# Kernel optimization log

Hardware: AMD Instinct MI355X
Metric: run time of the kernel (lower is better)

The kernel has to match this reference:

```python
import jax, jax.numpy as jnp
import numpy as np

B, V = 4, 5                      # batch_size, nview
CUBE = (80, 80, 20)              # PICT_STRUCT.CUBE_SIZE
NBINS = CUBE[0] * CUBE[1] * CUBE[2]
IMG_W, IMG_H = 960, 512          # NETWORK.IMAGE_SIZE (w, h)
ORI_W, ORI_H = 1920, 1080        # NETWORK.ORI_IMAGE_SIZE
HM_W, HM_H = 240, 128            # NETWORK.HEATMAP_SIZE
C_IMG, C_FEAT = 3, 32
C_TOT = C_IMG + C_FEAT
HID = 256
D_IN = 3 + 2 * C_TOT             # points + [mean, var] volume features


def setup_inputs():
    key = jax.random.key(0)
    ks = jax.random.split(key, 10)
    denorm_imgs = jax.random.uniform(ks[0], (V, B, C_IMG, IMG_H, IMG_W), jnp.float32)
    feats2d = jax.random.normal(ks[1], (V, B, C_FEAT, HM_H, HM_W), jnp.float32)
    lo = jnp.array([-1500.0, -1500.0, -300.0], jnp.float32)
    hi = jnp.array([1500.0, 1500.0, 300.0], jnp.float32)
    grids = lo + (hi - lo) * jax.random.uniform(ks[2], (B, NBINS, 3), jnp.float32)
    # near-identity rotations, camera centers ~3m behind the volume so all
    # points project inside the original image
    R = jnp.tile(jnp.eye(3, dtype=jnp.float32), (V, B, 1, 1)) \
        + 0.01 * jax.random.normal(ks[3], (V, B, 3, 3), jnp.float32)
    T = jnp.tile(jnp.array([0.0, 0.0, -3000.0], jnp.float32).reshape(3, 1), (V, B, 1, 1)) \
        + 50.0 * jax.random.normal(ks[4], (V, B, 3, 1), jnp.float32)
    f = 1500.0 + 10.0 * jax.random.normal(ks[5], (V, B, 2), jnp.float32)
    c_cam = jnp.tile(jnp.array([ORI_W / 2.0, ORI_H / 2.0], jnp.float32), (V, B, 1))
    k_dist = jnp.zeros((V, B, 3), jnp.float32)
    p_dist = jnp.zeros((V, B, 2), jnp.float32)
    resize_transform = jnp.array([[IMG_W / ORI_W, 0.0, 0.0],
                                  [0.0, IMG_H / ORI_H, 0.0]], jnp.float32)
    s1, s2 = 1.0 / np.sqrt(D_IN), 1.0 / np.sqrt(HID)
    W1 = (s1 * jax.random.normal(ks[6], (D_IN, HID))).astype(jnp.float32)
    b1 = jnp.zeros((HID,), jnp.float32)
    W2 = (s2 * jax.random.normal(ks[7], (HID, HID))).astype(jnp.float32)
    b2 = jnp.zeros((HID,), jnp.float32)
    W3 = (s2 * jax.random.normal(ks[8], (HID, 1))).astype(jnp.float32)
    b3 = jnp.zeros((1,), jnp.float32)
    return dict(denorm_imgs=denorm_imgs, feats2d=feats2d, grids=grids, R=R, T=T,
                f=f, c_cam=c_cam, k_dist=k_dist, p_dist=p_dist,
                resize_transform=resize_transform,
                W1=W1, b1=b1, W2=W2, b2=b2, W3=W3, b3=b3)


def _project(x, R, T, f, c, k, p):
    # voxelpose project_point_radial: x [N,3] world-mm -> [N,2] pixel coords
    xcam = R @ (x.T - T)                               # [3,N]
    y = xcam[:2] / (xcam[2:3] + 1e-5)                  # [2,N]
    r2 = jnp.sum(y * y, axis=0)
    radial = 1.0 + k[0] * r2 + k[1] * r2 ** 2 + k[2] * r2 ** 3
    tan = p[0] * y[1] + p[1] * y[0]
    y = y * (radial + 2.0 * tan)[None, :] + jnp.stack([p[1], p[0]])[:, None] * r2[None, :]
    return (f[:, None] * y + c[:, None]).T             # [N,2]


def _bilinear(img, gx, gy):
    # F.grid_sample bilinear, align_corners=True, padding_mode='zeros'
    # img: [C,H,W]; gx,gy: [N] in [-1,1] -> [C,N]
    C, H, W = img.shape
    x = (gx + 1.0) * 0.5 * (W - 1)
    y = (gy + 1.0) * 0.5 * (H - 1)
    x0, y0 = jnp.floor(x), jnp.floor(y)
    wx1, wy1 = x - x0, y - y0
    wx0, wy0 = 1.0 - wx1, 1.0 - wy1

    def tap(xi, yi):
        valid = (xi >= 0) & (xi <= W - 1) & (yi >= 0) & (yi <= H - 1)
        xi_c = jnp.clip(xi.astype(jnp.int32), 0, W - 1)
        yi_c = jnp.clip(yi.astype(jnp.int32), 0, H - 1)
        return img[:, yi_c, xi_c] * valid.astype(img.dtype)

    return (tap(x0, y0) * (wx0 * wy0) + tap(x0 + 1.0, y0) * (wx1 * wy0)
            + tap(x0, y0 + 1.0) * (wx0 * wy1) + tap(x0 + 1.0, y0 + 1.0) * (wx1 * wy1))


def _sample_view(img, feat, pts, R, T, f, c, k, p, trans):
    xy = _project(pts, R, T, f, c, k, p)
    xy = jnp.clip(xy, -1.0, float(max(ORI_W, ORI_H)))
    xy = jnp.concatenate([xy, jnp.ones((xy.shape[0], 1), xy.dtype)], axis=1) @ trans.T
    g = xy / jnp.array([IMG_W - 1.0, IMG_H - 1.0], jnp.float32) * 2.0 - 1.0
    si = _bilinear(img, g[:, 0], g[:, 1])              # [C_IMG, N]
    sf = _bilinear(feat, g[:, 0], g[:, 1])             # [C_FEAT, N]
    return jnp.concatenate([si, sf], axis=0)           # [C_TOT, N]


def reference(denorm_imgs, feats2d, grids, R, T, f, c_cam, k_dist, p_dist,
              resize_transform, W1, b1, W2, b2, W3, b3):
    per_b = jax.vmap(_sample_view, in_axes=(0, 0, 0, 0, 0, 0, 0, 0, 0, None))
    per_vb = jax.vmap(per_b, in_axes=(0, 0, None, 0, 0, 0, 0, 0, 0, None))
    cubes = per_vb(denorm_imgs, feats2d, grids, R, T, f, c_cam, k_dist, p_dist,
                   resize_transform)                   # [V,B,C,N]
    cubes = jnp.transpose(cubes, (1, 2, 3, 0))         # [B,C,N,V]
    mean = jnp.mean(cubes, axis=-1)                    # sum(cubes/nview)
    var = jnp.sum((cubes - mean[..., None]) ** 2, axis=-1) / V
    var = jnp.exp(-var)
    gvol = jnp.concatenate([mean, var], axis=1)        # [B,2C,N]
    # nerf_model.query_density: MLP over (points, per-point global volume feats)
    feat = jnp.concatenate([grids / 1000.0, jnp.swapaxes(gvol, 1, 2)], axis=-1)  # [B,N,D_IN]
    h = jax.nn.relu(feat @ W1 + b1)
    h = jax.nn.relu(h @ W2 + b2)
    density = jax.nn.softplus(h @ W3 + b3)             # [B,N,1]
    alpha = 1.0 - jnp.exp(-density)
    return alpha.reshape(B, 1, CUBE[0], CUBE[1], CUBE[2])
```

## Files before the change

### kernel.cpp

```cpp
#include <hip/hip_runtime.h>

#define NVIEW 5
#define BATCH 4
#define NPTS 128000
#define CIMG 3
#define CFEAT 32
#define CTOT 35
#define DIN 73
#define HID 256
#define IMG_W 960
#define IMG_H 512
#define HM_W 240
#define HM_H 128
#define HW_IMG (IMG_W * IMG_H)
#define HW_HM (HM_W * HM_H)

#define BP 32

typedef __attribute__((ext_vector_type(8))) short bf16x8;
typedef __attribute__((ext_vector_type(4))) float f32x4;
typedef __attribute__((ext_vector_type(4))) unsigned short ushort4v;
typedef __attribute__((ext_vector_type(8))) unsigned short ushort8v;

__device__ inline unsigned short bf16_rtne(float f) {
    unsigned u = __builtin_bit_cast(unsigned, f);
    u += 0x7FFFu + ((u >> 16) & 1u);
    return (unsigned short)(u >> 16);
}

struct Tap {
    int o00, o01, o10, o11;
    float w00, w01, w10, w11;
};

__device__ inline void make_tap(float gx, float gy, int W, int H, Tap& t) {
    float x = (gx + 1.0f) * 0.5f * (float)(W - 1);
    float y = (gy + 1.0f) * 0.5f * (float)(H - 1);
    float x0 = floorf(x), y0 = floorf(y);
    float x1 = x0 + 1.0f, y1 = y0 + 1.0f;
    float wx1 = x - x0, wy1 = y - y0;
    float wx0 = 1.0f - wx1, wy0 = 1.0f - wy1;
    float vx0 = (x0 >= 0.0f && x0 <= (float)(W - 1)) ? 1.0f : 0.0f;
    float vx1 = (x1 >= 0.0f && x1 <= (float)(W - 1)) ? 1.0f : 0.0f;
    float vy0 = (y0 >= 0.0f && y0 <= (float)(H - 1)) ? 1.0f : 0.0f;
    float vy1 = (y1 >= 0.0f && y1 <= (float)(H - 1)) ? 1.0f : 0.0f;
    int ix0 = min(max((int)x0, 0), W - 1);
    int ix1 = min(max((int)x1, 0), W - 1);
    int iy0 = min(max((int)y0, 0), H - 1);
    int iy1 = min(max((int)y1, 0), H - 1);
    t.o00 = iy0 * W + ix0;  t.w00 = wx0 * wy0 * vx0 * vy0;
    t.o01 = iy0 * W + ix1;  t.w01 = wx1 * wy0 * vx1 * vy0;
    t.o10 = iy1 * W + ix0;  t.w10 = wx0 * wy1 * vx0 * vy1;
    t.o11 = iy1 * W + ix1;  t.w11 = wx1 * wy1 * vx1 * vy1;
}

__device__ inline float4 f4zero() { float4 r; r.x = r.y = r.z = r.w = 0.f; return r; }
__device__ inline float4 f4fma(float w, float4 a, float4 acc) {
    acc.x += w * a.x; acc.y += w * a.y; acc.z += w * a.z; acc.w += w * a.w; return acc;
}
__device__ inline float4 f4add(float4 a, float4 b) {
    a.x += b.x; a.y += b.y; a.z += b.z; a.w += b.w; return a;
}
__device__ inline float4 f4addsq(float4 acc, float4 v) {
    acc.x += v.x * v.x; acc.y += v.y * v.y; acc.z += v.z * v.z; acc.w += v.w * v.w; return acc;
}

__global__ __launch_bounds__(256) void transpose_img(const float* __restrict__ in,
                                                     float* __restrict__ out) {
    int idx = blockIdx.x * 256 + threadIdx.x;
    int vb = idx / HW_IMG;
    int pix = idx - vb * HW_IMG;
    const float* src = in + (size_t)vb * 3 * HW_IMG + pix;
    float4 o;
    o.x = src[0];
    o.y = src[HW_IMG];
    o.z = src[2 * HW_IMG];
    o.w = 0.0f;
    reinterpret_cast<float4*>(out)[idx] = o;
}

__global__ __launch_bounds__(256) void transpose_feat(const float* __restrict__ in,
                                                      float* __restrict__ out) {
    int idx = blockIdx.x * 256 + threadIdx.x;
    int vb = idx / HW_HM;
    int pix = idx - vb * HW_HM;
    const float* src = in + (size_t)vb * 32 * HW_HM + pix;
    float4* dst = reinterpret_cast<float4*>(out) + (size_t)idx * 8;
#pragma unroll
    for (int k = 0; k < 8; ++k) {
        float4 o;
        o.x = src[(4 * k + 0) * HW_HM];
        o.y = src[(4 * k + 1) * HW_HM];
        o.z = src[(4 * k + 2) * HW_HM];
        o.w = src[(4 * k + 3) * HW_HM];
        dst[k] = o;
    }
}

__global__ __launch_bounds__(256) void prep_weights(const float* __restrict__ W1,
                                                    const float* __restrict__ W2,
                                                    unsigned short* __restrict__ W1b,
                                                    unsigned short* __restrict__ W2b) {
    int idx = blockIdx.x * 256 + threadIdx.x;
    if (idx < 16 * 3 * 64) {
        int l = idx & 63;
        int ks = (idx >> 6) % 3;
        int nt = idx / 192;
        int n = nt * 16 + (l & 15);
        int k0 = ks * 32 + (l >> 4) * 8;
        ushort8v o;
#pragma unroll
        for (int j = 0; j < 8; ++j) {
            int k = k0 + j;
            float v = (k < DIN) ? W1[k * HID + n] : 0.0f;
            o[j] = bf16_rtne(v);
        }
        reinterpret_cast<ushort8v*>(W1b)[idx] = o;
    } else if (idx < 16 * 3 * 64 + 16 * 8 * 64) {
        int id2 = idx - 16 * 3 * 64;
        int l = id2 & 63;
        int ks = (id2 >> 6) & 7;
        int nt = id2 >> 9;
        int n = nt * 16 + (l & 15);
        int k0 = ks * 32 + (l >> 4) * 8;
        ushort8v o;
#pragma unroll
        for (int j = 0; j < 8; ++j)
            o[j] = bf16_rtne(W2[(k0 + j) * HID + n]);
        reinterpret_cast<ushort8v*>(W2b)[id2] = o;
    }
}

__global__ __launch_bounds__(256, 4) void fused_denorm_project(
    const float* __restrict__ wsImg,
    const float* __restrict__ wsFeat,
    const unsigned short* __restrict__ W1b,
    const unsigned short* __restrict__ W2b,
    const float* __restrict__ grids,
    const float* __restrict__ Rm,
    const float* __restrict__ Tm,
    const float* __restrict__ fcam,
    const float* __restrict__ ccam,
    const float* __restrict__ kdist,
    const float* __restrict__ pdist,
    const float* __restrict__ trans,
    const float* __restrict__ b1,
    const float* __restrict__ b2,
    const float* __restrict__ W3,
    const float* __restrict__ b3,
    float* __restrict__ out)
{
    __shared__ unsigned short featb[BP * 96];
    __shared__ unsigned short h1T[BP * 256];
    __shared__ float b1L[HID], b2L[HID], w3L[HID];
    __shared__ float partial[4][BP];

    const int tid = threadIdx.x;
    const int blk = blockIdx.x;
    const int b   = blk / (NPTS / BP);
    const int n0  = (blk % (NPTS / BP)) * BP;

    b1L[tid] = b1[tid];
    b2L[tid] = b2[tid];
    w3L[tid] = W3[tid];

    {
        const int t = tid & 7;
        const int p = tid >> 3;
        const int n = n0 + p;
        char* fbB = (char*)featb;
        const int rowoff = p * 192;
        const int sw = (p & 7) << 4;

        const float px = grids[(b * NPTS + n) * 3 + 0];
        const float py = grids[(b * NPTS + n) * 3 + 1];
        const float pz = grids[(b * NPTS + n) * 3 + 2];
        if (t == 1) {
            *(unsigned short*)(fbB + ((rowoff + 0) ^ sw)) = bf16_rtne(px * 1e-3f);
            *(unsigned short*)(fbB + ((rowoff + 2) ^ sw)) = bf16_rtne(py * 1e-3f);
            *(unsigned short*)(fbB + ((rowoff + 4) ^ sw)) = bf16_rtne(pz * 1e-3f);
        }
        {
            int c0 = 73 + t * 3;
            int cnt = (t == 7) ? 2 : 3;
            for (int j = 0; j < cnt; ++j)
                *(unsigned short*)(fbB + ((rowoff + (c0 + j) * 2) ^ sw)) = 0;
        }
        const float t00 = trans[0], t01 = trans[1], t02 = trans[2];
        const float t10 = trans[3], t11 = trans[4], t12 = trans[5];

        float4 s4 = f4zero(), q4 = f4zero();
        float4 si = f4zero(), qi = f4zero();

        for (int v = 0; v < NVIEW; ++v) {
            const int vb = v * BATCH + b;
            const float* Rp = Rm + vb * 9;
            const float* Tp = Tm + vb * 3;
            float X = px - Tp[0], Y = py - Tp[1], Z = pz - Tp[2];
            float xc = Rp[0] * X + Rp[1] * Y + Rp[2] * Z;
            float yc = Rp[3] * X + Rp[4] * Y + Rp[5] * Z;
            float zc = Rp[6] * X + Rp[7] * Y + Rp[8] * Z;
            float inv = 1.0f / (zc + 1e-5f);
            float y0 = xc * inv, y1 = yc * inv;
            float r2 = y0 * y0 + y1 * y1;
            float k0 = kdist[vb * 3 + 0], k1 = kdist[vb * 3 + 1], k2 = kdist[vb * 3 + 2];
            float p0 = pdist[vb * 2 + 0], p1 = pdist[vb * 2 + 1];
            float radial = 1.0f + r2 * (k0 + r2 * (k1 + r2 * k2));
            float tn = p0 * y1 + p1 * y0;
            float scl = radial + 2.0f * tn;
            float uu = y0 * scl + p1 * r2;
            float vv = y1 * scl + p0 * r2;
            float xo = fcam[vb * 2 + 0] * uu + ccam[vb * 2 + 0];
            float yo = fcam[vb * 2 + 1] * vv + ccam[vb * 2 + 1];
            xo = fminf(fmaxf(xo, -1.0f), 1920.0f);
            yo = fminf(fmaxf(yo, -1.0f), 1920.0f);
            float xr = t00 * xo + t01 * yo + t02;
            float yr = t10 * xo + t11 * yo + t12;
            float gx = xr * (1.0f / (float)(IMG_W - 1)) * 2.0f - 1.0f;
            float gy = yr * (1.0f / (float)(IMG_H - 1)) * 2.0f - 1.0f;

            Tap tF;
            make_tap(gx, gy, HM_W, HM_H, tF);
            const float4* fb = reinterpret_cast<const float4*>(
                wsFeat + (size_t)vb * HW_HM * 32) + t;
            float4 a00 = fb[tF.o00 * 8];
            float4 a01 = fb[tF.o01 * 8];
            float4 a10 = fb[tF.o10 * 8];
            float4 a11 = fb[tF.o11 * 8];
            float4 val = f4zero();
            val = f4fma(tF.w00, a00, val);
            val = f4fma(tF.w01, a01, val);
            val = f4fma(tF.w10, a10, val);
            val = f4fma(tF.w11, a11, val);
            s4 = f4add(s4, val);
            q4 = f4addsq(q4, val);

            if (t == 0) {
                Tap tI;
                make_tap(gx, gy, IMG_W, IMG_H, tI);
                const float4* ib = reinterpret_cast<const float4*>(
                    wsImg + (size_t)vb * HW_IMG * 4);
                float4 i00 = ib[tI.o00];
                float4 i01 = ib[tI.o01];
                float4 i10 = ib[tI.o10];
                float4 i11 = ib[tI.o11];
                float4 vi = f4zero();
                vi = f4fma(tI.w00, i00, vi);
                vi = f4fma(tI.w01, i01, vi);
                vi = f4fma(tI.w10, i10, vi);
                vi = f4fma(tI.w11, i11, vi);
                si = f4add(si, vi);
                qi = f4addsq(qi, vi);
            }
        }

        const float inv5 = 1.0f / (float)NVIEW;
        {
            float m0 = s4.x * inv5, m1 = s4.y * inv5, m2 = s4.z * inv5, m3 = s4.w * inv5;
            int cm = 6 + 4 * t;
            int cv = 41 + 4 * t;
            *(unsigned short*)(fbB + ((rowoff + (cm + 0) * 2) ^ sw)) = bf16_rtne(m0);
            *(unsigned short*)(fbB + ((rowoff + (cm + 1) * 2) ^ sw)) = bf16_rtne(m1);
            *(unsigned short*)(fbB + ((rowoff + (cm + 2) * 2) ^ sw)) = bf16_rtne(m2);
            *(unsigned short*)(fbB + ((rowoff + (cm + 3) * 2) ^ sw)) = bf16_rtne(m3);
            *(unsigned short*)(fbB + ((rowoff + (cv + 0) * 2) ^ sw)) = bf16_rtne(expf(-(q4.x * inv5 - m0 * m0)));
            *(unsigned short*)(fbB + ((rowoff + (cv + 1) * 2) ^ sw)) = bf16_rtne(expf(-(q4.y * inv5 - m1 * m1)));
            *(unsigned short*)(fbB + ((rowoff + (cv + 2) * 2) ^ sw)) = bf16_rtne(expf(-(q4.z * inv5 - m2 * m2)));
            *(unsigned short*)(fbB + ((rowoff + (cv + 3) * 2) ^ sw)) = bf16_rtne(expf(-(q4.w * inv5 - m3 * m3)));
        }
        if (t == 0) {
            float m0 = si.x * inv5, m1 = si.y * inv5, m2 = si.z * inv5;
            *(unsigned short*)(fbB + ((rowoff + 3 * 2) ^ sw)) = bf16_rtne(m0);
            *(unsigned short*)(fbB + ((rowoff + 4 * 2) ^ sw)) = bf16_rtne(m1);
            *(unsigned short*)(fbB + ((rowoff + 5 * 2) ^ sw)) = bf16_rtne(m2);
            *(unsigned short*)(fbB + ((rowoff + 38 * 2) ^ sw)) = bf16_rtne(expf(-(qi.x * inv5 - m0 * m0)));
            *(unsigned short*)(fbB + ((rowoff + 39 * 2) ^ sw)) = bf16_rtne(expf(-(qi.y * inv5 - m1 * m1)));
            *(unsigned short*)(fbB + ((rowoff + 40 * 2) ^ sw)) = bf16_rtne(expf(-(qi.z * inv5 - m2 * m2)));
        }
    }
    __syncthreads();

    const int l   = tid & 63;
    const int w   = tid >> 6;
    const int g   = l >> 4;
    const int c16 = l & 15;

    {
        f32x4 acc[4][2];
#pragma unroll
        for (int nl = 0; nl < 4; ++nl)
#pragma unroll
            for (int pt = 0; pt < 2; ++pt) acc[nl][pt] = (f32x4)0.0f;

        const bf16x8* wfrag = reinterpret_cast<const bf16x8*>(W1b);
#pragma unroll
        for (int ks = 0; ks < 3; ++ks) {
            bf16x8 bfr[2];
#pragma unroll
            for (int pt = 0; pt < 2; ++pt) {
                int p = pt * 16 + c16;
                int off = (p * 192 + (ks * 32 + g * 8) * 2) ^ ((p & 7) << 4);
                bfr[pt] = *reinterpret_cast<const bf16x8*>((const char*)featb + off);
            }
#pragma unroll
            for (int nl = 0; nl < 4; ++nl) {
                int nt = w * 4 + nl;
                bf16x8 a = wfrag[(nt * 3 + ks) * 64 + l];
                acc[nl][0] = __builtin_amdgcn_mfma_f32_16x16x32_bf16(a, bfr[0], acc[nl][0], 0, 0, 0);
                acc[nl][1] = __builtin_amdgcn_mfma_f32_16x16x32_bf16(a, bfr[1], acc[nl][1], 0, 0, 0);
            }
        }
#pragma unroll
        for (int nl = 0; nl < 4; ++nl) {
            int nb = (w * 4 + nl) * 16 + g * 4;
            float bb0 = b1L[nb + 0], bb1 = b1L[nb + 1], bb2 = b1L[nb + 2], bb3v = b1L[nb + 3];
#pragma unroll
            for (int pt = 0; pt < 2; ++pt) {
                int p = pt * 16 + c16;
                ushort4v pk;
                pk[0] = bf16_rtne(fmaxf(acc[nl][pt][0] + bb0, 0.0f));
                pk[1] = bf16_rtne(fmaxf(acc[nl][pt][1] + bb1, 0.0f));
                pk[2] = bf16_rtne(fmaxf(acc[nl][pt][2] + bb2, 0.0f));
                pk[3] = bf16_rtne(fmaxf(acc[nl][pt][3] + bb3v, 0.0f));
                int off = (p * 512 + nb * 2) ^ ((p & 7) << 4);
                *reinterpret_cast<ushort4v*>((char*)h1T + off) = pk;
            }
        }
    }
    __syncthreads();

    {
        f32x4 acc[4][2];
#pragma unroll
        for (int nl = 0; nl < 4; ++nl)
#pragma unroll
            for (int pt = 0; pt < 2; ++pt) acc[nl][pt] = (f32x4)0.0f;

        const bf16x8* wfrag = reinterpret_cast<const bf16x8*>(W2b);
#pragma unroll
        for (int ks = 0; ks < 8; ++ks) {
            bf16x8 bfr[2];
#pragma unroll
            for (int pt = 0; pt < 2; ++pt) {
                int p = pt * 16 + c16;
                int off = (p * 512 + (ks * 32 + g * 8) * 2) ^ ((p & 7) << 4);
                bfr[pt] = *reinterpret_cast<const bf16x8*>((const char*)h1T + off);
            }
#pragma unroll
            for (int nl = 0; nl < 4; ++nl) {
                int nt = w * 4 + nl;
                bf16x8 a = wfrag[(nt * 8 + ks) * 64 + l];
                acc[nl][0] = __builtin_amdgcn_mfma_f32_16x16x32_bf16(a, bfr[0], acc[nl][0], 0, 0, 0);
                acc[nl][1] = __builtin_amdgcn_mfma_f32_16x16x32_bf16(a, bfr[1], acc[nl][1], 0, 0, 0);
            }
        }
        float s0 = 0.0f, s1 = 0.0f;
#pragma unroll
        for (int nl = 0; nl < 4; ++nl) {
            int nb = (w * 4 + nl) * 16 + g * 4;
#pragma unroll
            for (int r = 0; r < 4; ++r) {
                float b2v = b2L[nb + r];
                float w3v = w3L[nb + r];
                s0 += fmaxf(acc[nl][0][r] + b2v, 0.0f) * w3v;
                s1 += fmaxf(acc[nl][1][r] + b2v, 0.0f) * w3v;
            }
        }
        s0 += __shfl_xor(s0, 16, 64);
        s0 += __shfl_xor(s0, 32, 64);
        s1 += __shfl_xor(s1, 16, 64);
        s1 += __shfl_xor(s1, 32, 64);
        if (g == 0) {
            partial[w][c16]      = s0;
            partial[w][16 + c16] = s1;
        }
    }
    __syncthreads();

    if (tid < BP) {
        float v = partial[0][tid] + partial[1][tid] + partial[2][tid] + partial[3][tid] + b3[0];
        out[b * NPTS + n0 + tid] = 1.0f / (1.0f + expf(-v));
    }
}

extern "C" void kernel_launch(void* const* d_in, const int* in_sizes, int n_in,
                              void* d_out, int out_size, void* d_ws, size_t ws_size,
                              hipStream_t stream) {
    const float* imgs  = (const float*)d_in[0];
    const float* feats = (const float*)d_in[1];
    const float* grids = (const float*)d_in[2];
    const float* Rm    = (const float*)d_in[3];
    const float* Tm    = (const float*)d_in[4];
    const float* fcam  = (const float*)d_in[5];
    const float* ccam  = (const float*)d_in[6];
    const float* kdist = (const float*)d_in[7];
    const float* pdist = (const float*)d_in[8];
    const float* trans = (const float*)d_in[9];
    const float* W1    = (const float*)d_in[10];
    const float* b1    = (const float*)d_in[11];
    const float* W2    = (const float*)d_in[12];
    const float* b2    = (const float*)d_in[13];
    const float* W3    = (const float*)d_in[14];
    const float* b3    = (const float*)d_in[15];
    float* out = (float*)d_out;

    float* wsImg  = (float*)d_ws;
    float* wsFeat = wsImg + (size_t)NVIEW * BATCH * HW_IMG * 4;
    unsigned short* W1b = (unsigned short*)(wsFeat + (size_t)NVIEW * BATCH * HW_HM * 32);
    unsigned short* W2b = W1b + 16 * 3 * 64 * 8;

    transpose_img<<<(NVIEW * BATCH * HW_IMG) / 256, 256, 0, stream>>>(imgs, wsImg);
    transpose_feat<<<(NVIEW * BATCH * HW_HM) / 256, 256, 0, stream>>>(feats, wsFeat);
    prep_weights<<<44, 256, 0, stream>>>(W1, W2, W1b, W2b);

    const int nblocks = BATCH * (NPTS / BP);
    fused_denorm_project<<<nblocks, 256, 0, stream>>>(
        wsImg, wsFeat, W1b, W2b, grids, Rm, Tm, fcam, ccam, kdist, pdist, trans,
        b1, b2, W3, b3, out);
}
```

Baseline: 564.7 us.

## Store sampled image and feature maps as bf16 and share per-view taps via shuffles

The channel-last image and feature workspaces are now written as bf16 instead of fp32, which halves gather traffic in the fused kernel and write traffic in the transpose kernels. The image transpose also uses vectorized float4 loads, four pixels per thread. Each lane t<5 of an 8-lane group computes the projection and bilinear taps for one view, and the other lanes fetch them with __shfl instead of recomputing them. Image sampling is spread across five lanes and reduced with xor shuffles, rather than done serially by lane 0. Inputs lose precision by being rounded to bf16 before interpolation.

```diff
diff --git a/kernel.cpp b/kernel.cpp
--- a/kernel.cpp
+++ b/kernel.cpp
@@ -26,6 +26,9 @@
     unsigned u = __builtin_bit_cast(unsigned, f);
     u += 0x7FFFu + ((u >> 16) & 1u);
     return (unsigned short)(u >> 16);
+}
+__device__ inline float bf2f(unsigned short u) {
+    return __builtin_bit_cast(float, ((unsigned)u) << 16);
 }
 
 struct Tap {
@@ -55,8 +58,9 @@
 }
 
 __device__ inline float4 f4zero() { float4 r; r.x = r.y = r.z = r.w = 0.f; return r; }
-__device__ inline float4 f4fma(float w, float4 a, float4 acc) {
-    acc.x += w * a.x; acc.y += w * a.y; acc.z += w * a.z; acc.w += w * a.w; return acc;
+__device__ inline float4 tapacc(ushort4v a, float w, float4 acc) {
+    acc.x += w * bf2f(a[0]); acc.y += w * bf2f(a[1]);
+    acc.z += w * bf2f(a[2]); acc.w += w * bf2f(a[3]); return acc;
 }
 __device__ inline float4 f4add(float4 a, float4 b) {
     a.x += b.x; a.y += b.y; a.z += b.z; a.w += b.w; return a;
@@ -66,33 +70,37 @@
 }
 
 __global__ __launch_bounds__(256) void transpose_img(const float* __restrict__ in,
-                                                     float* __restrict__ out) {
+                                                     unsigned short* __restrict__ out) {
     int idx = blockIdx.x * 256 + threadIdx.x;
-    int vb = idx / HW_IMG;
-    int pix = idx - vb * HW_IMG;
-    const float* src = in + (size_t)vb * 3 * HW_IMG + pix;
-    float4 o;
-    o.x = src[0];
-    o.y = src[HW_IMG];
-    o.z = src[2 * HW_IMG];
-    o.w = 0.0f;
-    reinterpret_cast<float4*>(out)[idx] = o;
+    int vb = idx / (HW_IMG / 4);
+    int p4 = idx - vb * (HW_IMG / 4);
+    const float* src = in + (size_t)vb * 3 * HW_IMG + p4 * 4;
+    float4 c0 = *reinterpret_cast<const float4*>(src);
+    float4 c1 = *reinterpret_cast<const float4*>(src + HW_IMG);
+    float4 c2 = *reinterpret_cast<const float4*>(src + 2 * HW_IMG);
+    ushort8v o01, o23;
+    o01[0] = bf16_rtne(c0.x); o01[1] = bf16_rtne(c1.x); o01[2] = bf16_rtne(c2.x); o01[3] = 0;
+    o01[4] = bf16_rtne(c0.y); o01[5] = bf16_rtne(c1.y); o01[6] = bf16_rtne(c2.y); o01[7] = 0;
+    o23[0] = bf16_rtne(c0.z); o23[1] = bf16_rtne(c1.z); o23[2] = bf16_rtne(c2.z); o23[3] = 0;
+    o23[4] = bf16_rtne(c0.w); o23[5] = bf16_rtne(c1.w); o23[6] = bf16_rtne(c2.w); o23[7] = 0;
+    ushort8v* dst = reinterpret_cast<ushort8v*>(out + ((size_t)vb * HW_IMG + p4 * 4) * 4);
+    dst[0] = o01;
+    dst[1] = o23;
 }
 
 __global__ __launch_bounds__(256) void transpose_feat(const float* __restrict__ in,
-                                                      float* __restrict__ out) {
+                                                      unsigned short* __restrict__ out) {
     int idx = blockIdx.x * 256 + threadIdx.x;
     int vb = idx / HW_HM;
     int pix = idx - vb * HW_HM;
     const float* src = in + (size_t)vb * 32 * HW_HM + pix;
-    float4* dst = reinterpret_cast<float4*>(out) + (size_t)idx * 8;
-#pragma unroll
-    for (int k = 0; k < 8; ++k) {
-        float4 o;
-        o.x = src[(4 * k + 0) * HW_HM];
-        o.y = src[(4 * k + 1) * HW_HM];
-        o.z = src[(4 * k + 2) * HW_HM];
-        o.w = src[(4 * k + 3) * HW_HM];
+    ushort8v* dst = reinterpret_cast<ushort8v*>(out + (size_t)idx * 32);
+#pragma unroll
+    for (int k = 0; k < 4; ++k) {
+        ushort8v o;
+#pragma unroll
+        for (int j = 0; j < 8; ++j)
+            o[j] = bf16_rtne(src[(8 * k + j) * HW_HM]);
         dst[k] = o;
     }
 }
@@ -132,8 +140,8 @@
 }
 
 __global__ __launch_bounds__(256, 4) void fused_denorm_project(
-    const float* __restrict__ wsImg,
-    const float* __restrict__ wsFeat,
+    const unsigned short* __restrict__ wsImg,
+    const unsigned short* __restrict__ wsFeat,
     const unsigned short* __restrict__ W1b,
     const unsigned short* __restrict__ W2b,
     const float* __restrict__ grids,
@@ -186,14 +194,10 @@
             for (int j = 0; j < cnt; ++j)
                 *(unsigned short*)(fbB + ((rowoff + (c0 + j) * 2) ^ sw)) = 0;
         }
-        const float t00 = trans[0], t01 = trans[1], t02 = trans[2];
-        const float t10 = trans[3], t11 = trans[4], t12 = trans[5];
-
-        float4 s4 = f4zero(), q4 = f4zero();
-        float4 si = f4zero(), qi = f4zero();
-
-        for (int v = 0; v < NVIEW; ++v) {
-            const int vb = v * BATCH + b;
+
+        Tap myF = {}; Tap myI = {};
+        if (t < NVIEW) {
+            const int vb = t * BATCH + b;
             const float* Rp = Rm + vb * 9;
             const float* Tp = Tm + vb * 3;
             float X = px - Tp[0], Y = py - Tp[1], Z = pz - Tp[2];
@@ -214,44 +218,64 @@
             float yo = fcam[vb * 2 + 1] * vv + ccam[vb * 2 + 1];
             xo = fminf(fmaxf(xo, -1.0f), 1920.0f);
             yo = fminf(fmaxf(yo, -1.0f), 1920.0f);
-            float xr = t00 * xo + t01 * yo + t02;
-            float yr = t10 * xo + t11 * yo + t12;
+            float xr = trans[0] * xo + trans[1] * yo + trans[2];
+            float yr = trans[3] * xo + trans[4] * yo + trans[5];
             float gx = xr * (1.0f / (float)(IMG_W - 1)) * 2.0f - 1.0f;
             float gy = yr * (1.0f / (float)(IMG_H - 1)) * 2.0f - 1.0f;
-
+            make_tap(gx, gy, HM_W, HM_H, myF);
+            make_tap(gx, gy, IMG_W, IMG_H, myI);
+        }
+
+        float4 s4 = f4zero(), q4 = f4zero();
+        const int lb = (tid & 63) & 56;
+        for (int v = 0; v < NVIEW; ++v) {
+            const int src = lb + v;
             Tap tF;
-            make_tap(gx, gy, HM_W, HM_H, tF);
-            const float4* fb = reinterpret_cast<const float4*>(
-                wsFeat + (size_t)vb * HW_HM * 32) + t;
-            float4 a00 = fb[tF.o00 * 8];
-            float4 a01 = fb[tF.o01 * 8];
-            float4 a10 = fb[tF.o10 * 8];
-            float4 a11 = fb[tF.o11 * 8];
+            tF.o00 = __shfl(myF.o00, src, 64);
+            tF.o01 = __shfl(myF.o01, src, 64);
+            tF.o10 = __shfl(myF.o10, src, 64);
+            tF.o11 = __shfl(myF.o11, src, 64);
+            tF.w00 = __shfl(myF.w00, src, 64);
+            tF.w01 = __shfl(myF.w01, src, 64);
+            tF.w10 = __shfl(myF.w10, src, 64);
+            tF.w11 = __shfl(myF.w11, src, 64);
+            const unsigned short* fb = wsFeat + (size_t)(v * BATCH + b) * HW_HM * 32 + t * 4;
+            ushort4v a00 = *reinterpret_cast<const ushort4v*>(fb + (size_t)tF.o00 * 32);
+            ushort4v a01 = *reinterpret_cast<const ushort4v*>(fb + (size_t)tF.o01 * 32);
+            ushort4v a10 = *reinterpret_cast<const ushort4v*>(fb + (size_t)tF.o10 * 32);
+            ushort4v a11 = *reinterpret_cast<const ushort4v*>(fb + (size_t)tF.o11 * 32);
             float4 val = f4zero();
-            val = f4fma(tF.w00, a00, val);
-            val = f4fma(tF.w01, a01, val);
-            val = f4fma(tF.w10, a10, val);
-            val = f4fma(tF.w11, a11, val);
+            val = tapacc(a00, tF.w00, val);
+            val = tapacc(a01, tF.w01, val);
+            val = tapacc(a10, tF.w10, val);
+            val = tapacc(a11, tF.w11, val);
             s4 = f4add(s4, val);
             q4 = f4addsq(q4, val);
-
-            if (t == 0) {
-                Tap tI;
-                make_tap(gx, gy, IMG_W, IMG_H, tI);
-                const float4* ib = reinterpret_cast<const float4*>(
-                    wsImg + (size_t)vb * HW_IMG * 4);
-                float4 i00 = ib[tI.o00];
-                float4 i01 = ib[tI.o01];
-                float4 i10 = ib[tI.o10];
-                float4 i11 = ib[tI.o11];
-                float4 vi = f4zero();
-                vi = f4fma(tI.w00, i00, vi);
-                vi = f4fma(tI.w01, i01, vi);
-                vi = f4fma(tI.w10, i10, vi);
-                vi = f4fma(tI.w11, i11, vi);
-                si = f4add(si, vi);
-                qi = f4addsq(qi, vi);
-            }
+        }
+
+        float4 si = f4zero(), qi = f4zero();
+        if (t < NVIEW) {
+            const unsigned short* ib = wsImg + (size_t)(t * BATCH + b) * HW_IMG * 4;
+            ushort4v i00 = *reinterpret_cast<const ushort4v*>(ib + (size_t)myI.o00 * 4);
+            ushort4v i01 = *reinterpret_cast<const ushort4v*>(ib + (size_t)myI.o01 * 4);
+            ushort4v i10 = *reinterpret_cast<const ushort4v*>(ib + (size_t)myI.o10 * 4);
+            ushort4v i11 = *reinterpret_cast<const ushort4v*>(ib + (size_t)myI.o11 * 4);
+            float4 vi = f4zero();
+            vi = tapacc(i00, myI.w00, vi);
+            vi = tapacc(i01, myI.w01, vi);
+            vi = tapacc(i10, myI.w10, vi);
+            vi = tapacc(i11, myI.w11, vi);
+            si = vi;
+            qi = f4addsq(f4zero(), vi);
+        }
+#pragma unroll
+        for (int off = 1; off <= 4; off <<= 1) {
+            si.x += __shfl_xor(si.x, off, 64);
+            si.y += __shfl_xor(si.y, off, 64);
+            si.z += __shfl_xor(si.z, off, 64);
+            qi.x += __shfl_xor(qi.x, off, 64);
+            qi.y += __shfl_xor(qi.y, off, 64);
+            qi.z += __shfl_xor(qi.z, off, 64);
         }
 
         const float inv5 = 1.0f / (float)NVIEW;
@@ -404,12 +428,12 @@
     const float* b3    = (const float*)d_in[15];
     float* out = (float*)d_out;
 
-    float* wsImg  = (float*)d_ws;
-    float* wsFeat = wsImg + (size_t)NVIEW * BATCH * HW_IMG * 4;
-    unsigned short* W1b = (unsigned short*)(wsFeat + (size_t)NVIEW * BATCH * HW_HM * 32);
-    unsigned short* W2b = W1b + 16 * 3 * 64 * 8;
-
-    transpose_img<<<(NVIEW * BATCH * HW_IMG) / 256, 256, 0, stream>>>(imgs, wsImg);
+    unsigned short* wsImg  = (unsigned short*)d_ws;
+    unsigned short* wsFeat = wsImg + (size_t)NVIEW * BATCH * HW_IMG * 4;
+    unsigned short* W1b    = wsFeat + (size_t)NVIEW * BATCH * HW_HM * 32;
+    unsigned short* W2b    = W1b + 16 * 3 * 64 * 8;
+
+    transpose_img<<<(NVIEW * BATCH * HW_IMG / 4) / 256, 256, 0, stream>>>(imgs, wsImg);
     transpose_feat<<<(NVIEW * BATCH * HW_HM) / 256, 256, 0, stream>>>(feats, wsFeat);
     prep_weights<<<44, 256, 0, stream>>>(W1, W2, W1b, W2b);
 
```

Measured after the change: 509.0 us. -9.9%, faster.
